# Kernel tuning notes

Hardware: AMD Instinct MI355X
Metric: run time of the kernel (lower is better)

Reference implementation:

```python
import jax, jax.numpy as jnp
import numpy as np

PATCH = 16  # conv kernel size == stride


def _patch_embed(im, W, b):
    # im: (B, C, H, W) NCHW; W: (hidden, C, s, s); returns (B, h, w, hidden)
    out = jax.lax.conv_general_dilated(
        im, W, window_strides=(PATCH, PATCH), padding='VALID',
        dimension_numbers=('NCHW', 'OIHW', 'NCHW'))
    out = out + b[None, :, None, None]
    return jnp.transpose(out, (0, 2, 3, 1))  # (B, h, w, hidden)


def setup_inputs() -> dict:
    key = jax.random.key(0)
    k1, k2, k3, k4 = jax.random.split(key, 4)
    B, C, H, Wd = 64, 3, 224, 224
    hidden = 384
    x = jax.random.normal(k1, (B, C, H, Wd), dtype=jnp.float32)
    y = jax.random.normal(k2, (B, C, H, Wd), dtype=jnp.float32)
    fan_in = C * PATCH * PATCH
    bound = 1.0 / np.sqrt(fan_in)
    W = jax.random.uniform(k3, (hidden, C, PATCH, PATCH), dtype=jnp.float32,
                           minval=-bound, maxval=bound)
    b = jax.random.uniform(k4, (hidden,), dtype=jnp.float32,
                           minval=-bound, maxval=bound)
    return {'x': x, 'y': y, 'W': W, 'b': b}


def reference(x, y, W, b):
    B = x.shape[0]
    xp = _patch_embed(x, W, b)  # (B, h, w, C)
    yp = _patch_embed(y, W, b)  # (B, h, w, C)
    h, w = xp.shape[1], xp.shape[2]
    logp = jax.nn.log_softmax(xp, axis=-1)          # (B, h, w, C)
    q = jax.lax.stop_gradient(jax.nn.softmax(yp, axis=-1))  # detached targets
    # CE[i, j] = mean over (h, w) of -(q_j * logp_i).sum(-1)
    # Faithful factorization of the (B, B, h, w, C) broadcast in the original.
    CE = -jnp.einsum('ihwc,jhwc->ij', logp, q) / (h * w)  # (B, B)
    close = jnp.trace(CE) / B
    far = (CE.sum() - jnp.trace(CE)) / (B * B - B)
    return close / far
```

## Files before the change

### kernel.cpp

```cpp
#include <hip/hip_runtime.h>

#define HID   384
#define K_PE  768
#define IMGST 150528

typedef unsigned short ushort_t;
using f32x4  = __attribute__((ext_vector_type(4))) float;
using short8 = __attribute__((ext_vector_type(8))) short;

__device__ __forceinline__ unsigned bfpack(float lo, float hi) {
    union { float f; unsigned u; } a, b; a.f = lo; b.f = hi;
    unsigned ra = (a.u + 0x7fffu + ((a.u >> 16) & 1u)) >> 16;
    unsigned rb = (b.u + 0x7fffu + ((b.u >> 16) & 1u)) & 0xffff0000u;
    return ra | rb;
}

__global__ __launch_bounds__(256) void prep(const float* __restrict__ W,
                                            ushort_t* __restrict__ Wfrag,
                                            float* __restrict__ scal) {
    const int t = blockIdx.x * 256 + threadIdx.x;
    if (t < 4) scal[t] = 0.f;
    const int n  = t / 96;
    const int ko = t % 96;
    const float4 a = *(const float4*)(W + (size_t)n * K_PE + ko * 8);
    const float4 b = *(const float4*)(W + (size_t)n * K_PE + ko * 8 + 4);
    uint4 p;
    p.x = bfpack(a.x, a.y); p.y = bfpack(a.z, a.w);
    p.z = bfpack(b.x, b.y); p.w = bfpack(b.z, b.w);
    const int nt   = n >> 4;
    const int kc   = ko >> 2;
    const int lane = (ko & 3) * 16 + (n & 15);
    ((uint4*)Wfrag)[(nt * 24 + kc) * 64 + lane] = p;
}

__global__ __launch_bounds__(512, 2) void pe_all(
    const float* __restrict__ xin, const float* __restrict__ yin,
    const ushort_t* __restrict__ Wfrag, const float* __restrict__ bias,
    float* __restrict__ scal, float* __restrict__ out) {
    const int p  = blockIdx.x;
    const int pi = p / 14;
    const int pj = p - pi * 14;

    __shared__ __align__(16) ushort_t Asx[2][64 * 64];
    __shared__ __align__(16) ushort_t Asy[2][64 * 64];
    __shared__ float Smx[8][32], Ssx[8][32], Smy[8][32], Ssy[8][32];
    __shared__ float LcL[2][HID], LcQ[2][HID];
    __shared__ float sT[8], sS[8];

    const int tid  = threadIdx.x;
    const int wave = tid >> 6;
    const int lane = tid & 63;
    const int lm   = lane & 15;
    const int lq   = lane >> 4;
    const int mg   = wave >> 2;
    const int nw   = wave & 3;
    const int wn   = nw * 96;

    const int sm = tid >> 3;
    const int qt = tid & 7;
    const float* abx = xin + (size_t)sm * IMGST + pi * 3584 + pj * 16;
    const float* aby = yin + (size_t)sm * IMGST + pi * 3584 + pj * 16;
    const int awoff = sm * 64 + ((qt ^ (sm & 7)) * 8);

    int ard[2][2];
#pragma unroll
    for (int ks = 0; ks < 2; ++ks)
#pragma unroll
        for (int mi = 0; mi < 2; ++mi)
            ard[ks][mi] = (mg * 32 + mi * 16 + lm) * 64 +
                          (((ks * 4 + lq) ^ (lm & 7)) * 8);

    const ushort_t* bbase = Wfrag + (size_t)lane * 8;

    f32x4 accx[2][6] = {};
    f32x4 accy[2][6] = {};

#define STAGE(KB, BUF)                                                       \
    {                                                                        \
        const int k0  = (KB) + qt * 8;                                       \
        const int off = (k0 >> 8) * 50176 + (((k0 >> 4) & 15) * 224) + (k0 & 15); \
        float4 f0 = *(const float4*)(abx + off);                             \
        float4 f1 = *(const float4*)(abx + off + 4);                         \
        float4 g0 = *(const float4*)(aby + off);                             \
        float4 g1 = *(const float4*)(aby + off + 4);                         \
        uint4 px, py;                                                        \
        px.x = bfpack(f0.x, f0.y); px.y = bfpack(f0.z, f0.w);                \
        px.z = bfpack(f1.x, f1.y); px.w = bfpack(f1.z, f1.w);                \
        py.x = bfpack(g0.x, g0.y); py.y = bfpack(g0.z, g0.w);                \
        py.z = bfpack(g1.x, g1.y); py.w = bfpack(g1.z, g1.w);                \
        *(uint4*)&Asx[BUF][awoff] = px;                                      \
        *(uint4*)&Asy[BUF][awoff] = py;                                      \
    }

    STAGE(0, 0)
    __syncthreads();

    for (int kbi = 0; kbi < 12; ++kbi) {
        const int cur = kbi & 1;
        if (kbi < 11) STAGE(kbi * 64 + 64, cur ^ 1)
#pragma unroll
        for (int ks = 0; ks < 2; ++ks) {
            short8 bfr[6], afx[2], afy[2];
#pragma unroll
            for (int ni = 0; ni < 6; ++ni)
                bfr[ni] = *(const short8*)(bbase +
                          (size_t)(((nw * 6 + ni) * 24 + kbi * 2 + ks) * 64) * 8);
#pragma unroll
            for (int mi = 0; mi < 2; ++mi) {
                afx[mi] = *(const short8*)&Asx[cur][ard[ks][mi]];
                afy[mi] = *(const short8*)&Asy[cur][ard[ks][mi]];
            }
#pragma unroll
            for (int mi = 0; mi < 2; ++mi)
#pragma unroll
                for (int ni = 0; ni < 6; ++ni) {
                    accx[mi][ni] = __builtin_amdgcn_mfma_f32_16x16x32_bf16(
                        afx[mi], bfr[ni], accx[mi][ni], 0, 0, 0);
                    accy[mi][ni] = __builtin_amdgcn_mfma_f32_16x16x32_bf16(
                        afy[mi], bfr[ni], accy[mi][ni], 0, 0, 0);
                }
        }
        __syncthreads();
    }
#undef STAGE

#pragma unroll
    for (int ni = 0; ni < 6; ++ni) {
        const float bv = bias[wn + ni * 16 + lm];
#pragma unroll
        for (int mi = 0; mi < 2; ++mi)
#pragma unroll
            for (int r = 0; r < 4; ++r) {
                accx[mi][ni][r] += bv;
                accy[mi][ni][r] += bv;
            }
    }

    float mx[2][4], my_[2][4];
#pragma unroll
    for (int mi = 0; mi < 2; ++mi)
#pragma unroll
        for (int r = 0; r < 4; ++r) {
            float a = accx[mi][0][r], b = accy[mi][0][r];
#pragma unroll
            for (int ni = 1; ni < 6; ++ni) {
                a = fmaxf(a, accx[mi][ni][r]);
                b = fmaxf(b, accy[mi][ni][r]);
            }
            mx[mi][r] = a; my_[mi][r] = b;
        }
#pragma unroll
    for (int off = 1; off < 16; off <<= 1)
#pragma unroll
        for (int mi = 0; mi < 2; ++mi)
#pragma unroll
            for (int r = 0; r < 4; ++r) {
                mx[mi][r]  = fmaxf(mx[mi][r],  __shfl_xor(mx[mi][r],  off));
                my_[mi][r] = fmaxf(my_[mi][r], __shfl_xor(my_[mi][r], off));
            }
    if (lm == 0)
#pragma unroll
        for (int mi = 0; mi < 2; ++mi)
#pragma unroll
            for (int r = 0; r < 4; ++r) {
                Smx[wave][mi * 16 + lq * 4 + r] = mx[mi][r];
                Smy[wave][mi * 16 + lq * 4 + r] = my_[mi][r];
            }
    __syncthreads();
#pragma unroll
    for (int mi = 0; mi < 2; ++mi)
#pragma unroll
        for (int r = 0; r < 4; ++r) {
            const int row = mi * 16 + lq * 4 + r;
            mx[mi][r]  = fmaxf(fmaxf(Smx[mg * 4 + 0][row], Smx[mg * 4 + 1][row]),
                               fmaxf(Smx[mg * 4 + 2][row], Smx[mg * 4 + 3][row]));
            my_[mi][r] = fmaxf(fmaxf(Smy[mg * 4 + 0][row], Smy[mg * 4 + 1][row]),
                               fmaxf(Smy[mg * 4 + 2][row], Smy[mg * 4 + 3][row]));
        }

    float sx[2][4], sy[2][4];
#pragma unroll
    for (int mi = 0; mi < 2; ++mi)
#pragma unroll
        for (int r = 0; r < 4; ++r) {
            float a = 0.f, b = 0.f;
#pragma unroll
            for (int ni = 0; ni < 6; ++ni) {
                a += __expf(accx[mi][ni][r] - mx[mi][r]);
                b += __expf(accy[mi][ni][r] - my_[mi][r]);
            }
            sx[mi][r] = a; sy[mi][r] = b;
        }
#pragma unroll
    for (int off = 1; off < 16; off <<= 1)
#pragma unroll
        for (int mi = 0; mi < 2; ++mi)
#pragma unroll
            for (int r = 0; r < 4; ++r) {
                sx[mi][r] += __shfl_xor(sx[mi][r], off);
                sy[mi][r] += __shfl_xor(sy[mi][r], off);
            }
    if (lm == 0)
#pragma unroll
        for (int mi = 0; mi < 2; ++mi)
#pragma unroll
            for (int r = 0; r < 4; ++r) {
                Ssx[wave][mi * 16 + lq * 4 + r] = sx[mi][r];
                Ssy[wave][mi * 16 + lq * 4 + r] = sy[mi][r];
            }
    __syncthreads();
#pragma unroll
    for (int mi = 0; mi < 2; ++mi)
#pragma unroll
        for (int r = 0; r < 4; ++r) {
            const int row = mi * 16 + lq * 4 + r;
            const float ssx = Ssx[mg * 4 + 0][row] + Ssx[mg * 4 + 1][row] +
                              Ssx[mg * 4 + 2][row] + Ssx[mg * 4 + 3][row];
            const float ssy = Ssy[mg * 4 + 0][row] + Ssy[mg * 4 + 1][row] +
                              Ssy[mg * 4 + 2][row] + Ssy[mg * 4 + 3][row];
            sx[mi][r] = mx[mi][r] + __logf(ssx);
            sy[mi][r] = 1.f / ssy;
        }

    float T = 0.f;
    float cL[6], cQ[6];
#pragma unroll
    for (int ni = 0; ni < 6; ++ni) { cL[ni] = 0.f; cQ[ni] = 0.f; }
#pragma unroll
    for (int mi = 0; mi < 2; ++mi)
#pragma unroll
        for (int r = 0; r < 4; ++r) {
            const float sh  = sx[mi][r];
            const float m   = my_[mi][r];
            const float inv = sy[mi][r];
#pragma unroll
            for (int ni = 0; ni < 6; ++ni) {
                const float lp = accx[mi][ni][r] - sh;
                const float qv = __expf(accy[mi][ni][r] - m) * inv;
                T += lp * qv;
                cL[ni] += lp;
                cQ[ni] += qv;
            }
        }
#pragma unroll
    for (int ni = 0; ni < 6; ++ni) {
        cL[ni] += __shfl_xor(cL[ni], 16); cL[ni] += __shfl_xor(cL[ni], 32);
        cQ[ni] += __shfl_xor(cQ[ni], 16); cQ[ni] += __shfl_xor(cQ[ni], 32);
    }
    if (lq == 0)
#pragma unroll
        for (int ni = 0; ni < 6; ++ni) {
            LcL[mg][wn + ni * 16 + lm] = cL[ni];
            LcQ[mg][wn + ni * 16 + lm] = cQ[ni];
        }
#pragma unroll
    for (int off = 32; off > 0; off >>= 1) T += __shfl_xor(T, off);
    if (lane == 0) sT[wave] = T;
    __syncthreads();

    float sp = 0.f;
    if (tid < HID) {
        const float L = LcL[0][tid] + LcL[1][tid];
        const float Q = LcQ[0][tid] + LcQ[1][tid];
        sp = L * Q;
    }
#pragma unroll
    for (int off = 32; off > 0; off >>= 1) sp += __shfl_xor(sp, off);
    if (lane == 0) sS[wave] = sp;
    __syncthreads();

    if (tid == 0) {
        float Tb = sT[0] + sT[1] + sT[2] + sT[3] + sT[4] + sT[5] + sT[6] + sT[7];
        float Sb = sS[0] + sS[1] + sS[2] + sS[3] + sS[4] + sS[5] + sS[6] + sS[7];
        atomicAdd(&scal[0], Tb);
        atomicAdd(&scal[1], Sb);
        __threadfence();
        int old = atomicAdd((int*)&scal[3], 1);
        if (old == (int)gridDim.x - 1) {
            float Tt = atomicAdd(&scal[0], 0.f);
            float St = atomicAdd(&scal[1], 0.f);
            out[0] = 63.f * Tt / (St - Tt);
        }
    }
}

extern "C" void kernel_launch(void* const* d_in, const int* in_sizes, int n_in,
                              void* d_out, int out_size, void* d_ws, size_t ws_size,
                              hipStream_t stream) {
    const float* x = (const float*)d_in[0];
    const float* y = (const float*)d_in[1];
    const float* W = (const float*)d_in[2];
    const float* b = (const float*)d_in[3];
    float* out = (float*)d_out;

    float*    scal  = (float*)d_ws;
    ushort_t* Wfrag = (ushort_t*)(scal + 16);

    prep<<<144, 256, 0, stream>>>(W, Wfrag, scal);
    pe_all<<<196, 512, 0, stream>>>(x, y, Wfrag, b, scal, out);
}
```

Before: 146.2 us.

## Split patch-embed blocks over batch sub-tiles and add a reduction kernel

The main kernel now launches four times as many smaller blocks: each block handles 16 batch rows of one patch position with 256 threads instead of all 64 rows with 512 threads. The goal is to fill more of the CUs than 196 large blocks can. Per-channel column sums of logp and q are written to global scratch, and a new finish kernel combines the four sub-blocks, forms the L·Q cross term and computes the final ratio. Staging is also changed so each thread loads one matrix (x or y) and the bf16 pack plus LDS store happen after the MFMAs, which hides global-load latency. In exchange there is an extra kernel launch and scratch traffic, and every weight fragment is reloaded by four times as many blocks.

```diff
diff --git a/kernel.cpp b/kernel.cpp
--- a/kernel.cpp
+++ b/kernel.cpp
@@ -3,6 +3,7 @@
 #define HID   384
 #define K_PE  768
 #define IMGST 150528
+#define MSUB  16
 
 typedef unsigned short ushort_t;
 using f32x4  = __attribute__((ext_vector_type(4))) float;
@@ -33,215 +34,187 @@
     ((uint4*)Wfrag)[(nt * 24 + kc) * 64 + lane] = p;
 }
 
-__global__ __launch_bounds__(512, 2) void pe_all(
+__global__ __launch_bounds__(256, 3) void pe_all(
     const float* __restrict__ xin, const float* __restrict__ yin,
     const ushort_t* __restrict__ Wfrag, const float* __restrict__ bias,
-    float* __restrict__ scal, float* __restrict__ out) {
-    const int p  = blockIdx.x;
-    const int pi = p / 14;
-    const int pj = p - pi * 14;
-
-    __shared__ __align__(16) ushort_t Asx[2][64 * 64];
-    __shared__ __align__(16) ushort_t Asy[2][64 * 64];
-    __shared__ float Smx[8][32], Ssx[8][32], Smy[8][32], Ssy[8][32];
-    __shared__ float LcL[2][HID], LcQ[2][HID];
-    __shared__ float sT[8], sS[8];
+    float* __restrict__ scal, float* __restrict__ Lg, float* __restrict__ Qg) {
+    const int blk = blockIdx.x;
+    const int p   = blk >> 2;
+    const int sub = blk & 3;
+    const int pi  = p / 14;
+    const int pj  = p - pi * 14;
+
+    __shared__ __align__(16) ushort_t Asx[2][MSUB * 64];
+    __shared__ __align__(16) ushort_t Asy[2][MSUB * 64];
+    __shared__ float Smx[4][16], Ssx[4][16], Smy[4][16], Ssy[4][16];
+    __shared__ float sT[4];
 
     const int tid  = threadIdx.x;
     const int wave = tid >> 6;
     const int lane = tid & 63;
     const int lm   = lane & 15;
     const int lq   = lane >> 4;
-    const int mg   = wave >> 2;
-    const int nw   = wave & 3;
-    const int wn   = nw * 96;
-
-    const int sm = tid >> 3;
-    const int qt = tid & 7;
-    const float* abx = xin + (size_t)sm * IMGST + pi * 3584 + pj * 16;
-    const float* aby = yin + (size_t)sm * IMGST + pi * 3584 + pj * 16;
-    const int awoff = sm * 64 + ((qt ^ (sm & 7)) * 8);
-
-    int ard[2][2];
+
+    const int mat  = tid >> 7;
+    const int sidx = tid & 127;
+    const int srow = sidx & 15;
+    const int soct = sidx >> 4;
+    const float* sbase = (mat ? yin : xin) +
+        (size_t)(sub * MSUB + srow) * IMGST + pi * 3584 + pj * 16;
+    ushort_t (* const Adst)[MSUB * 64] = mat ? Asy : Asx;
+    const int woff = srow * 64 + ((soct ^ (srow & 7)) * 8);
+
+    int ard[2];
 #pragma unroll
     for (int ks = 0; ks < 2; ++ks)
-#pragma unroll
-        for (int mi = 0; mi < 2; ++mi)
-            ard[ks][mi] = (mg * 32 + mi * 16 + lm) * 64 +
-                          (((ks * 4 + lq) ^ (lm & 7)) * 8);
+        ard[ks] = lm * 64 + (((ks * 4 + lq) ^ (lm & 7)) * 8);
 
     const ushort_t* bbase = Wfrag + (size_t)lane * 8;
 
-    f32x4 accx[2][6] = {};
-    f32x4 accy[2][6] = {};
-
-#define STAGE(KB, BUF)                                                       \
-    {                                                                        \
-        const int k0  = (KB) + qt * 8;                                       \
-        const int off = (k0 >> 8) * 50176 + (((k0 >> 4) & 15) * 224) + (k0 & 15); \
-        float4 f0 = *(const float4*)(abx + off);                             \
-        float4 f1 = *(const float4*)(abx + off + 4);                         \
-        float4 g0 = *(const float4*)(aby + off);                             \
-        float4 g1 = *(const float4*)(aby + off + 4);                         \
-        uint4 px, py;                                                        \
-        px.x = bfpack(f0.x, f0.y); px.y = bfpack(f0.z, f0.w);                \
-        px.z = bfpack(f1.x, f1.y); px.w = bfpack(f1.z, f1.w);                \
-        py.x = bfpack(g0.x, g0.y); py.y = bfpack(g0.z, g0.w);                \
-        py.z = bfpack(g1.x, g1.y); py.w = bfpack(g1.z, g1.w);                \
-        *(uint4*)&Asx[BUF][awoff] = px;                                      \
-        *(uint4*)&Asy[BUF][awoff] = py;                                      \
-    }
-
-    STAGE(0, 0)
+    f32x4 accx[6] = {};
+    f32x4 accy[6] = {};
+
+    {
+        const int k0  = soct * 8;
+        const int off = (k0 >> 8) * 50176 + (((k0 >> 4) & 15) * 224) + (k0 & 15);
+        const float4 f0 = *(const float4*)(sbase + off);
+        const float4 f1 = *(const float4*)(sbase + off + 4);
+        uint4 px;
+        px.x = bfpack(f0.x, f0.y); px.y = bfpack(f0.z, f0.w);
+        px.z = bfpack(f1.x, f1.y); px.w = bfpack(f1.z, f1.w);
+        *(uint4*)&Adst[0][woff] = px;
+    }
     __syncthreads();
 
     for (int kbi = 0; kbi < 12; ++kbi) {
         const int cur = kbi & 1;
-        if (kbi < 11) STAGE(kbi * 64 + 64, cur ^ 1)
+        const int kn  = (kbi < 11) ? (kbi + 1) * 64 + soct * 8 : soct * 8;
+        const int off = (kn >> 8) * 50176 + (((kn >> 4) & 15) * 224) + (kn & 15);
+        const float4 f0 = *(const float4*)(sbase + off);
+        const float4 f1 = *(const float4*)(sbase + off + 4);
+
 #pragma unroll
         for (int ks = 0; ks < 2; ++ks) {
-            short8 bfr[6], afx[2], afy[2];
+            short8 bfr[6];
 #pragma unroll
             for (int ni = 0; ni < 6; ++ni)
                 bfr[ni] = *(const short8*)(bbase +
-                          (size_t)(((nw * 6 + ni) * 24 + kbi * 2 + ks) * 64) * 8);
-#pragma unroll
-            for (int mi = 0; mi < 2; ++mi) {
-                afx[mi] = *(const short8*)&Asx[cur][ard[ks][mi]];
-                afy[mi] = *(const short8*)&Asy[cur][ard[ks][mi]];
+                          (size_t)(((wave * 6 + ni) * 24 + kbi * 2 + ks) * 64) * 8);
+            const short8 afx = *(const short8*)&Asx[cur][ard[ks]];
+            const short8 afy = *(const short8*)&Asy[cur][ard[ks]];
+#pragma unroll
+            for (int ni = 0; ni < 6; ++ni) {
+                accx[ni] = __builtin_amdgcn_mfma_f32_16x16x32_bf16(
+                    afx, bfr[ni], accx[ni], 0, 0, 0);
+                accy[ni] = __builtin_amdgcn_mfma_f32_16x16x32_bf16(
+                    afy, bfr[ni], accy[ni], 0, 0, 0);
             }
-#pragma unroll
-            for (int mi = 0; mi < 2; ++mi)
-#pragma unroll
-                for (int ni = 0; ni < 6; ++ni) {
-                    accx[mi][ni] = __builtin_amdgcn_mfma_f32_16x16x32_bf16(
-                        afx[mi], bfr[ni], accx[mi][ni], 0, 0, 0);
-                    accy[mi][ni] = __builtin_amdgcn_mfma_f32_16x16x32_bf16(
-                        afy[mi], bfr[ni], accy[mi][ni], 0, 0, 0);
-                }
-        }
+        }
+
+        uint4 px;
+        px.x = bfpack(f0.x, f0.y); px.y = bfpack(f0.z, f0.w);
+        px.z = bfpack(f1.x, f1.y); px.w = bfpack(f1.z, f1.w);
+        *(uint4*)&Adst[cur ^ 1][woff] = px;
         __syncthreads();
     }
-#undef STAGE
 
 #pragma unroll
     for (int ni = 0; ni < 6; ++ni) {
-        const float bv = bias[wn + ni * 16 + lm];
-#pragma unroll
-        for (int mi = 0; mi < 2; ++mi)
-#pragma unroll
-            for (int r = 0; r < 4; ++r) {
-                accx[mi][ni][r] += bv;
-                accy[mi][ni][r] += bv;
-            }
-    }
-
-    float mx[2][4], my_[2][4];
-#pragma unroll
-    for (int mi = 0; mi < 2; ++mi)
-#pragma unroll
-        for (int r = 0; r < 4; ++r) {
-            float a = accx[mi][0][r], b = accy[mi][0][r];
-#pragma unroll
-            for (int ni = 1; ni < 6; ++ni) {
-                a = fmaxf(a, accx[mi][ni][r]);
-                b = fmaxf(b, accy[mi][ni][r]);
-            }
-            mx[mi][r] = a; my_[mi][r] = b;
-        }
+        const float bv = bias[wave * 96 + ni * 16 + lm];
+#pragma unroll
+        for (int r = 0; r < 4; ++r) {
+            accx[ni][r] += bv;
+            accy[ni][r] += bv;
+        }
+    }
+
+    float mx[4], my_[4];
+#pragma unroll
+    for (int r = 0; r < 4; ++r) {
+        float a = accx[0][r], b = accy[0][r];
+#pragma unroll
+        for (int ni = 1; ni < 6; ++ni) {
+            a = fmaxf(a, accx[ni][r]);
+            b = fmaxf(b, accy[ni][r]);
+        }
+        mx[r] = a; my_[r] = b;
+    }
 #pragma unroll
     for (int off = 1; off < 16; off <<= 1)
 #pragma unroll
-        for (int mi = 0; mi < 2; ++mi)
-#pragma unroll
-            for (int r = 0; r < 4; ++r) {
-                mx[mi][r]  = fmaxf(mx[mi][r],  __shfl_xor(mx[mi][r],  off));
-                my_[mi][r] = fmaxf(my_[mi][r], __shfl_xor(my_[mi][r], off));
-            }
+        for (int r = 0; r < 4; ++r) {
+            mx[r]  = fmaxf(mx[r],  __shfl_xor(mx[r],  off));
+            my_[r] = fmaxf(my_[r], __shfl_xor(my_[r], off));
+        }
     if (lm == 0)
 #pragma unroll
-        for (int mi = 0; mi < 2; ++mi)
-#pragma unroll
-            for (int r = 0; r < 4; ++r) {
-                Smx[wave][mi * 16 + lq * 4 + r] = mx[mi][r];
-                Smy[wave][mi * 16 + lq * 4 + r] = my_[mi][r];
-            }
-    __syncthreads();
-#pragma unroll
-    for (int mi = 0; mi < 2; ++mi)
-#pragma unroll
-        for (int r = 0; r < 4; ++r) {
-            const int row = mi * 16 + lq * 4 + r;
-            mx[mi][r]  = fmaxf(fmaxf(Smx[mg * 4 + 0][row], Smx[mg * 4 + 1][row]),
-                               fmaxf(Smx[mg * 4 + 2][row], Smx[mg * 4 + 3][row]));
-            my_[mi][r] = fmaxf(fmaxf(Smy[mg * 4 + 0][row], Smy[mg * 4 + 1][row]),
-                               fmaxf(Smy[mg * 4 + 2][row], Smy[mg * 4 + 3][row]));
-        }
-
-    float sx[2][4], sy[2][4];
-#pragma unroll
-    for (int mi = 0; mi < 2; ++mi)
-#pragma unroll
-        for (int r = 0; r < 4; ++r) {
-            float a = 0.f, b = 0.f;
-#pragma unroll
-            for (int ni = 0; ni < 6; ++ni) {
-                a += __expf(accx[mi][ni][r] - mx[mi][r]);
-                b += __expf(accy[mi][ni][r] - my_[mi][r]);
-            }
-            sx[mi][r] = a; sy[mi][r] = b;
-        }
+        for (int r = 0; r < 4; ++r) {
+            Smx[wave][lq * 4 + r] = mx[r];
+            Smy[wave][lq * 4 + r] = my_[r];
+        }
+    __syncthreads();
+#pragma unroll
+    for (int r = 0; r < 4; ++r) {
+        const int row = lq * 4 + r;
+        mx[r]  = fmaxf(fmaxf(Smx[0][row], Smx[1][row]),
+                       fmaxf(Smx[2][row], Smx[3][row]));
+        my_[r] = fmaxf(fmaxf(Smy[0][row], Smy[1][row]),
+                       fmaxf(Smy[2][row], Smy[3][row]));
+    }
+
+    float sx[4], sy[4];
+#pragma unroll
+    for (int r = 0; r < 4; ++r) {
+        float a = 0.f, b = 0.f;
+#pragma unroll
+        for (int ni = 0; ni < 6; ++ni) {
+            a += __expf(accx[ni][r] - mx[r]);
+            b += __expf(accy[ni][r] - my_[r]);
+        }
+        sx[r] = a; sy[r] = b;
+    }
 #pragma unroll
     for (int off = 1; off < 16; off <<= 1)
 #pragma unroll
-        for (int mi = 0; mi < 2; ++mi)
-#pragma unroll
-            for (int r = 0; r < 4; ++r) {
-                sx[mi][r] += __shfl_xor(sx[mi][r], off);
-                sy[mi][r] += __shfl_xor(sy[mi][r], off);
-            }
+        for (int r = 0; r < 4; ++r) {
+            sx[r] += __shfl_xor(sx[r], off);
+            sy[r] += __shfl_xor(sy[r], off);
+        }
     if (lm == 0)
 #pragma unroll
-        for (int mi = 0; mi < 2; ++mi)
-#pragma unroll
-            for (int r = 0; r < 4; ++r) {
-                Ssx[wave][mi * 16 + lq * 4 + r] = sx[mi][r];
-                Ssy[wave][mi * 16 + lq * 4 + r] = sy[mi][r];
-            }
-    __syncthreads();
-#pragma unroll
-    for (int mi = 0; mi < 2; ++mi)
-#pragma unroll
-        for (int r = 0; r < 4; ++r) {
-            const int row = mi * 16 + lq * 4 + r;
-            const float ssx = Ssx[mg * 4 + 0][row] + Ssx[mg * 4 + 1][row] +
-                              Ssx[mg * 4 + 2][row] + Ssx[mg * 4 + 3][row];
-            const float ssy = Ssy[mg * 4 + 0][row] + Ssy[mg * 4 + 1][row] +
-                              Ssy[mg * 4 + 2][row] + Ssy[mg * 4 + 3][row];
-            sx[mi][r] = mx[mi][r] + __logf(ssx);
-            sy[mi][r] = 1.f / ssy;
-        }
+        for (int r = 0; r < 4; ++r) {
+            Ssx[wave][lq * 4 + r] = sx[r];
+            Ssy[wave][lq * 4 + r] = sy[r];
+        }
+    __syncthreads();
+    float shx[4], invy[4];
+#pragma unroll
+    for (int r = 0; r < 4; ++r) {
+        const int row = lq * 4 + r;
+        const float ssx = Ssx[0][row] + Ssx[1][row] + Ssx[2][row] + Ssx[3][row];
+        const float ssy = Ssy[0][row] + Ssy[1][row] + Ssy[2][row] + Ssy[3][row];
+        shx[r]  = mx[r] + __logf(ssx);
+        invy[r] = 1.f / ssy;
+    }
 
     float T = 0.f;
     float cL[6], cQ[6];
 #pragma unroll
     for (int ni = 0; ni < 6; ++ni) { cL[ni] = 0.f; cQ[ni] = 0.f; }
 #pragma unroll
-    for (int mi = 0; mi < 2; ++mi)
-#pragma unroll
-        for (int r = 0; r < 4; ++r) {
-            const float sh  = sx[mi][r];
-            const float m   = my_[mi][r];
-            const float inv = sy[mi][r];
-#pragma unroll
-            for (int ni = 0; ni < 6; ++ni) {
-                const float lp = accx[mi][ni][r] - sh;
-                const float qv = __expf(accy[mi][ni][r] - m) * inv;
-                T += lp * qv;
-                cL[ni] += lp;
-                cQ[ni] += qv;
-            }
-        }
+    for (int r = 0; r < 4; ++r) {
+        const float sh  = shx[r];
+        const float m   = my_[r];
+        const float inv = invy[r];
+#pragma unroll
+        for (int ni = 0; ni < 6; ++ni) {
+            const float lp = accx[ni][r] - sh;
+            const float qv = __expf(accy[ni][r] - m) * inv;
+            T += lp * qv;
+            cL[ni] += lp;
+            cQ[ni] += qv;
+        }
+    }
 #pragma unroll
     for (int ni = 0; ni < 6; ++ni) {
         cL[ni] += __shfl_xor(cL[ni], 16); cL[ni] += __shfl_xor(cL[ni], 32);
@@ -250,36 +223,40 @@
     if (lq == 0)
 #pragma unroll
         for (int ni = 0; ni < 6; ++ni) {
-            LcL[mg][wn + ni * 16 + lm] = cL[ni];
-            LcQ[mg][wn + ni * 16 + lm] = cQ[ni];
+            Lg[(size_t)blk * HID + wave * 96 + ni * 16 + lm] = cL[ni];
+            Qg[(size_t)blk * HID + wave * 96 + ni * 16 + lm] = cQ[ni];
         }
 #pragma unroll
     for (int off = 32; off > 0; off >>= 1) T += __shfl_xor(T, off);
     if (lane == 0) sT[wave] = T;
     __syncthreads();
-
-    float sp = 0.f;
-    if (tid < HID) {
-        const float L = LcL[0][tid] + LcL[1][tid];
-        const float Q = LcQ[0][tid] + LcQ[1][tid];
-        sp = L * Q;
-    }
-#pragma unroll
-    for (int off = 32; off > 0; off >>= 1) sp += __shfl_xor(sp, off);
-    if (lane == 0) sS[wave] = sp;
-    __syncthreads();
-
-    if (tid == 0) {
-        float Tb = sT[0] + sT[1] + sT[2] + sT[3] + sT[4] + sT[5] + sT[6] + sT[7];
-        float Sb = sS[0] + sS[1] + sS[2] + sS[3] + sS[4] + sS[5] + sS[6] + sS[7];
-        atomicAdd(&scal[0], Tb);
-        atomicAdd(&scal[1], Sb);
+    if (tid == 0) atomicAdd(&scal[0], sT[0] + sT[1] + sT[2] + sT[3]);
+}
+
+__global__ __launch_bounds__(384) void finish(const float* __restrict__ Lg,
+                                              const float* __restrict__ Qg,
+                                              float* __restrict__ scal,
+                                              float* __restrict__ out) {
+    const int p = blockIdx.x;
+    const int c = threadIdx.x;
+    const size_t b0 = (size_t)(p * 4) * HID + c;
+    const float L = Lg[b0] + Lg[b0 + HID] + Lg[b0 + 2 * HID] + Lg[b0 + 3 * HID];
+    const float Q = Qg[b0] + Qg[b0 + HID] + Qg[b0 + 2 * HID] + Qg[b0 + 3 * HID];
+    float s = L * Q;
+#pragma unroll
+    for (int off = 32; off > 0; off >>= 1) s += __shfl_xor(s, off);
+    __shared__ float sw[6];
+    if ((c & 63) == 0) sw[c >> 6] = s;
+    __syncthreads();
+    if (c == 0) {
+        const float Sp = sw[0] + sw[1] + sw[2] + sw[3] + sw[4] + sw[5];
+        atomicAdd(&scal[1], Sp);
         __threadfence();
-        int old = atomicAdd((int*)&scal[3], 1);
-        if (old == (int)gridDim.x - 1) {
-            float Tt = atomicAdd(&scal[0], 0.f);
-            float St = atomicAdd(&scal[1], 0.f);
-            out[0] = 63.f * Tt / (St - Tt);
+        const int old = atomicAdd((int*)&scal[3], 1);
+        if (old == 195) {
+            const float T = atomicAdd(&scal[0], 0.f);
+            const float S = atomicAdd(&scal[1], 0.f);
+            out[0] = 63.f * T / (S - T);
         }
     }
 }
@@ -295,7 +272,10 @@
 
     float*    scal  = (float*)d_ws;
     ushort_t* Wfrag = (ushort_t*)(scal + 16);
+    float*    Lg    = (float*)(Wfrag + 294912);
+    float*    Qg    = Lg + (size_t)784 * HID;
 
     prep<<<144, 256, 0, stream>>>(W, Wfrag, scal);
-    pe_all<<<196, 512, 0, stream>>>(x, y, Wfrag, b, scal, out);
-}
+    pe_all<<<784, 256, 0, stream>>>(x, y, Wfrag, b, scal, Lg, Qg);
+    finish<<<196, 384, 0, stream>>>(Lg, Qg, scal, out);
+}
```

New measurement: 154.8 us. 1.06x slower.

## Pre-pack images to bf16 patch tiles and stream them into LDS asynchronously

Applied to the files above, without the earlier changes.

A new pack kernel converts both images to bf16 once, reading rows coalesced through shared memory, and writes them in a per-position, per-k-block tile layout. The main GEMM kernel then uses global_load_lds to copy these tiles straight into LDS. It also splits each patch position across two 256-thread blocks (392 blocks in total). Column sums are combined across the two halves with global atomics and a per-position last-block reduction. This replaces the strided fp32 gathers and the in-loop conversion, and gives more blocks for occupancy, at the cost of an extra write and read of about 38MB of bf16 data and extra atomics.

```diff
diff --git a/kernel.cpp b/kernel.cpp
--- a/kernel.cpp
+++ b/kernel.cpp
@@ -3,10 +3,18 @@
 #define HID   384
 #define K_PE  768
 #define IMGST 150528
+#define POS   196
 
 typedef unsigned short ushort_t;
 using f32x4  = __attribute__((ext_vector_type(4))) float;
 using short8 = __attribute__((ext_vector_type(8))) short;
+
+typedef unsigned __attribute__((address_space(1))) u32_g;
+typedef unsigned __attribute__((address_space(3))) u32_s;
+
+__device__ __forceinline__ void glds16(const void* g, void* l) {
+    __builtin_amdgcn_global_load_lds((const u32_g*)g, (u32_s*)l, 16, 0, 0);
+}
 
 __device__ __forceinline__ unsigned bfpack(float lo, float hi) {
     union { float f; unsigned u; } a, b; a.f = lo; b.f = hi;
@@ -15,81 +23,114 @@
     return ra | rb;
 }
 
-__global__ __launch_bounds__(256) void prep(const float* __restrict__ W,
-                                            ushort_t* __restrict__ Wfrag,
-                                            float* __restrict__ scal) {
-    const int t = blockIdx.x * 256 + threadIdx.x;
-    if (t < 4) scal[t] = 0.f;
-    const int n  = t / 96;
-    const int ko = t % 96;
-    const float4 a = *(const float4*)(W + (size_t)n * K_PE + ko * 8);
-    const float4 b = *(const float4*)(W + (size_t)n * K_PE + ko * 8 + 4);
-    uint4 p;
-    p.x = bfpack(a.x, a.y); p.y = bfpack(a.z, a.w);
-    p.z = bfpack(b.x, b.y); p.w = bfpack(b.z, b.w);
-    const int nt   = n >> 4;
-    const int kc   = ko >> 2;
-    const int lane = (ko & 3) * 16 + (n & 15);
-    ((uint4*)Wfrag)[(nt * 24 + kc) * 64 + lane] = p;
-}
-
-__global__ __launch_bounds__(512, 2) void pe_all(
-    const float* __restrict__ xin, const float* __restrict__ yin,
+__global__ __launch_bounds__(256) void pack(
+    const float* __restrict__ x, const float* __restrict__ y,
+    const float* __restrict__ W, ushort_t* __restrict__ Wfrag,
+    ushort_t* __restrict__ imx, ushort_t* __restrict__ imy,
+    float* __restrict__ scal, int* __restrict__ pcnt,
+    float* __restrict__ Lp, float* __restrict__ Qp) {
+    const int b   = blockIdx.x;
+    const int tid = threadIdx.x;
+
+    if (b >= 896) {
+        const int t = (b - 896) * 256 + tid;
+        if (t < 16)  scal[t] = 0.f;
+        if (t < POS) pcnt[t] = 0;
+        for (int i = t; i < POS * HID; i += 36864) { Lp[i] = 0.f; Qp[i] = 0.f; }
+        const int n  = t / 96;
+        const int ko = t - n * 96;
+        const float4 a  = *(const float4*)(W + (size_t)n * K_PE + ko * 8);
+        const float4 bb = *(const float4*)(W + (size_t)n * K_PE + ko * 8 + 4);
+        uint4 pq;
+        pq.x = bfpack(a.x, a.y);  pq.y = bfpack(a.z, a.w);
+        pq.z = bfpack(bb.x, bb.y); pq.w = bfpack(bb.z, bb.w);
+        const int nt    = n >> 4;
+        const int kc    = ko >> 2;
+        const int lanew = (ko & 3) * 16 + (n & 15);
+        ((uint4*)Wfrag)[(nt * 24 + kc) * 64 + lanew] = pq;
+        return;
+    }
+
+    const int pi  = b >> 6;
+    const int img = b & 63;
+    __shared__ __align__(16) ushort_t L[2][48 * 232];
+
+    const float* bx = x + (size_t)img * IMGST + pi * 3584;
+    const float* by = y + (size_t)img * IMGST + pi * 3584;
+
+    for (int i = tid; i < 2688; i += 256) {
+        const int row = i / 56;
+        const int c4  = i - row * 56;
+        const int c   = row >> 4, r = row & 15;
+        const size_t so = (size_t)c * 50176 + r * 224 + c4 * 4;
+        const float4 fx = *(const float4*)(bx + so);
+        const float4 fy = *(const float4*)(by + so);
+        uint2 px, py;
+        px.x = bfpack(fx.x, fx.y); px.y = bfpack(fx.z, fx.w);
+        py.x = bfpack(fy.x, fy.y); py.y = bfpack(fy.z, fy.w);
+        *(uint2*)&L[0][row * 232 + c4 * 4] = px;
+        *(uint2*)&L[1][row * 232 + c4 * 4] = py;
+    }
+    __syncthreads();
+
+    for (int u = tid; u < 1344; u += 256) {
+        const int pj  = u / 96;
+        const int oc  = u - pj * 96;
+        const int kbi = oc >> 3, o = oc & 7;
+        const int k0  = oc * 8;
+        const int c   = k0 >> 8, kh = (k0 >> 4) & 15, kw0 = k0 & 15;
+        const int loff = (c * 16 + kh) * 232 + pj * 16 + kw0;
+        const uint4 vx = *(const uint4*)&L[0][loff];
+        const uint4 vy = *(const uint4*)&L[1][loff];
+        const size_t d = ((size_t)((pi * 14 + pj) * 12 + kbi) * 64 + img) * 64 + o * 8;
+        *(uint4*)&imx[d] = vx;
+        *(uint4*)&imy[d] = vy;
+    }
+}
+
+__global__ __launch_bounds__(256, 3) void pe2(
+    const ushort_t* __restrict__ imx, const ushort_t* __restrict__ imy,
     const ushort_t* __restrict__ Wfrag, const float* __restrict__ bias,
-    float* __restrict__ scal, float* __restrict__ out) {
-    const int p  = blockIdx.x;
-    const int pi = p / 14;
-    const int pj = p - pi * 14;
-
-    __shared__ __align__(16) ushort_t Asx[2][64 * 64];
-    __shared__ __align__(16) ushort_t Asy[2][64 * 64];
-    __shared__ float Smx[8][32], Ssx[8][32], Smy[8][32], Ssy[8][32];
-    __shared__ float LcL[2][HID], LcQ[2][HID];
-    __shared__ float sT[8], sS[8];
+    float* __restrict__ scal, int* __restrict__ pcnt,
+    float* __restrict__ Lp, float* __restrict__ Qp, float* __restrict__ out) {
+    const int blk  = blockIdx.x;
+    const int p    = blk >> 1;
+    const int half = blk & 1;
+
+    __shared__ __align__(16) ushort_t As[2][4096];
+    __shared__ float Smx[4][32], Ssx[4][32], Smy[4][32], Ssy[4][32];
+    __shared__ float sT[4];
+    __shared__ int lastp;
 
     const int tid  = threadIdx.x;
     const int wave = tid >> 6;
     const int lane = tid & 63;
     const int lm   = lane & 15;
     const int lq   = lane >> 4;
-    const int mg   = wave >> 2;
-    const int nw   = wave & 3;
-    const int wn   = nw * 96;
-
-    const int sm = tid >> 3;
-    const int qt = tid & 7;
-    const float* abx = xin + (size_t)sm * IMGST + pi * 3584 + pj * 16;
-    const float* aby = yin + (size_t)sm * IMGST + pi * 3584 + pj * 16;
-    const int awoff = sm * 64 + ((qt ^ (sm & 7)) * 8);
+
+    const int simg = wave * 8 + (lane >> 3);
+    const int so   = (lane & 7) ^ ((lane >> 3) & 7);
+    const size_t sbyte = (size_t)p * 98304 +
+                         ((size_t)(half * 32 + simg)) * 128 + so * 16;
+    const char* gx = (const char*)imx + sbyte;
+    const char* gy = (const char*)imy + sbyte;
 
     int ard[2][2];
 #pragma unroll
     for (int ks = 0; ks < 2; ++ks)
 #pragma unroll
         for (int mi = 0; mi < 2; ++mi)
-            ard[ks][mi] = (mg * 32 + mi * 16 + lm) * 64 +
-                          (((ks * 4 + lq) ^ (lm & 7)) * 8);
+            ard[ks][mi] = (mi * 16 + lm) * 64 + (((ks * 4 + lq) ^ (lm & 7)) * 8);
 
     const ushort_t* bbase = Wfrag + (size_t)lane * 8;
 
     f32x4 accx[2][6] = {};
     f32x4 accy[2][6] = {};
 
-#define STAGE(KB, BUF)                                                       \
-    {                                                                        \
-        const int k0  = (KB) + qt * 8;                                       \
-        const int off = (k0 >> 8) * 50176 + (((k0 >> 4) & 15) * 224) + (k0 & 15); \
-        float4 f0 = *(const float4*)(abx + off);                             \
-        float4 f1 = *(const float4*)(abx + off + 4);                         \
-        float4 g0 = *(const float4*)(aby + off);                             \
-        float4 g1 = *(const float4*)(aby + off + 4);                         \
-        uint4 px, py;                                                        \
-        px.x = bfpack(f0.x, f0.y); px.y = bfpack(f0.z, f0.w);                \
-        px.z = bfpack(f1.x, f1.y); px.w = bfpack(f1.z, f1.w);                \
-        py.x = bfpack(g0.x, g0.y); py.y = bfpack(g0.z, g0.w);                \
-        py.z = bfpack(g1.x, g1.y); py.w = bfpack(g1.z, g1.w);                \
-        *(uint4*)&Asx[BUF][awoff] = px;                                      \
-        *(uint4*)&Asy[BUF][awoff] = py;                                      \
+#define STAGE(KB, BUF)                                       \
+    {                                                        \
+        glds16(gx + (size_t)(KB) * 8192, &As[BUF][wave * 512]);        \
+        glds16(gy + (size_t)(KB) * 8192, &As[BUF][2048 + wave * 512]); \
     }
 
     STAGE(0, 0)
@@ -97,18 +138,19 @@
 
     for (int kbi = 0; kbi < 12; ++kbi) {
         const int cur = kbi & 1;
-        if (kbi < 11) STAGE(kbi * 64 + 64, cur ^ 1)
 #pragma unroll
         for (int ks = 0; ks < 2; ++ks) {
-            short8 bfr[6], afx[2], afy[2];
+            short8 bfr[6];
 #pragma unroll
             for (int ni = 0; ni < 6; ++ni)
                 bfr[ni] = *(const short8*)(bbase +
-                          (size_t)(((nw * 6 + ni) * 24 + kbi * 2 + ks) * 64) * 8);
+                          (size_t)(((wave * 6 + ni) * 24 + kbi * 2 + ks) * 64) * 8);
+            if (ks == 0 && kbi < 11) STAGE(kbi + 1, cur ^ 1)
+            short8 afx[2], afy[2];
 #pragma unroll
             for (int mi = 0; mi < 2; ++mi) {
-                afx[mi] = *(const short8*)&Asx[cur][ard[ks][mi]];
-                afy[mi] = *(const short8*)&Asy[cur][ard[ks][mi]];
+                afx[mi] = *(const short8*)&As[cur][ard[ks][mi]];
+                afy[mi] = *(const short8*)&As[cur][2048 + ard[ks][mi]];
             }
 #pragma unroll
             for (int mi = 0; mi < 2; ++mi)
@@ -126,7 +168,7 @@
 
 #pragma unroll
     for (int ni = 0; ni < 6; ++ni) {
-        const float bv = bias[wn + ni * 16 + lm];
+        const float bv = bias[wave * 96 + ni * 16 + lm];
 #pragma unroll
         for (int mi = 0; mi < 2; ++mi)
 #pragma unroll
@@ -141,13 +183,13 @@
     for (int mi = 0; mi < 2; ++mi)
 #pragma unroll
         for (int r = 0; r < 4; ++r) {
-            float a = accx[mi][0][r], b = accy[mi][0][r];
+            float a = accx[mi][0][r], bb = accy[mi][0][r];
 #pragma unroll
             for (int ni = 1; ni < 6; ++ni) {
-                a = fmaxf(a, accx[mi][ni][r]);
-                b = fmaxf(b, accy[mi][ni][r]);
-            }
-            mx[mi][r] = a; my_[mi][r] = b;
+                a  = fmaxf(a,  accx[mi][ni][r]);
+                bb = fmaxf(bb, accy[mi][ni][r]);
+            }
+            mx[mi][r] = a; my_[mi][r] = bb;
         }
 #pragma unroll
     for (int off = 1; off < 16; off <<= 1)
@@ -172,10 +214,10 @@
 #pragma unroll
         for (int r = 0; r < 4; ++r) {
             const int row = mi * 16 + lq * 4 + r;
-            mx[mi][r]  = fmaxf(fmaxf(Smx[mg * 4 + 0][row], Smx[mg * 4 + 1][row]),
-                               fmaxf(Smx[mg * 4 + 2][row], Smx[mg * 4 + 3][row]));
-            my_[mi][r] = fmaxf(fmaxf(Smy[mg * 4 + 0][row], Smy[mg * 4 + 1][row]),
-                               fmaxf(Smy[mg * 4 + 2][row], Smy[mg * 4 + 3][row]));
+            mx[mi][r]  = fmaxf(fmaxf(Smx[0][row], Smx[1][row]),
+                               fmaxf(Smx[2][row], Smx[3][row]));
+            my_[mi][r] = fmaxf(fmaxf(Smy[0][row], Smy[1][row]),
+                               fmaxf(Smy[2][row], Smy[3][row]));
         }
 
     float sx[2][4], sy[2][4];
@@ -183,13 +225,13 @@
     for (int mi = 0; mi < 2; ++mi)
 #pragma unroll
         for (int r = 0; r < 4; ++r) {
-            float a = 0.f, b = 0.f;
+            float a = 0.f, bb = 0.f;
 #pragma unroll
             for (int ni = 0; ni < 6; ++ni) {
-                a += __expf(accx[mi][ni][r] - mx[mi][r]);
-                b += __expf(accy[mi][ni][r] - my_[mi][r]);
-            }
-            sx[mi][r] = a; sy[mi][r] = b;
+                a  += __expf(accx[mi][ni][r] - mx[mi][r]);
+                bb += __expf(accy[mi][ni][r] - my_[mi][r]);
+            }
+            sx[mi][r] = a; sy[mi][r] = bb;
         }
 #pragma unroll
     for (int off = 1; off < 16; off <<= 1)
@@ -209,17 +251,16 @@
                 Ssy[wave][mi * 16 + lq * 4 + r] = sy[mi][r];
             }
     __syncthreads();
+    float shx[2][4], invy[2][4];
 #pragma unroll
     for (int mi = 0; mi < 2; ++mi)
 #pragma unroll
         for (int r = 0; r < 4; ++r) {
             const int row = mi * 16 + lq * 4 + r;
-            const float ssx = Ssx[mg * 4 + 0][row] + Ssx[mg * 4 + 1][row] +
-                              Ssx[mg * 4 + 2][row] + Ssx[mg * 4 + 3][row];
-            const float ssy = Ssy[mg * 4 + 0][row] + Ssy[mg * 4 + 1][row] +
-                              Ssy[mg * 4 + 2][row] + Ssy[mg * 4 + 3][row];
-            sx[mi][r] = mx[mi][r] + __logf(ssx);
-            sy[mi][r] = 1.f / ssy;
+            const float ssx = Ssx[0][row] + Ssx[1][row] + Ssx[2][row] + Ssx[3][row];
+            const float ssy = Ssy[0][row] + Ssy[1][row] + Ssy[2][row] + Ssy[3][row];
+            shx[mi][r]  = mx[mi][r] + __logf(ssx);
+            invy[mi][r] = 1.f / ssy;
         }
 
     float T = 0.f;
@@ -230,9 +271,9 @@
     for (int mi = 0; mi < 2; ++mi)
 #pragma unroll
         for (int r = 0; r < 4; ++r) {
-            const float sh  = sx[mi][r];
+            const float sh  = shx[mi][r];
             const float m   = my_[mi][r];
-            const float inv = sy[mi][r];
+            const float inv = invy[mi][r];
 #pragma unroll
             for (int ni = 0; ni < 6; ++ni) {
                 const float lp = accx[mi][ni][r] - sh;
@@ -250,35 +291,41 @@
     if (lq == 0)
 #pragma unroll
         for (int ni = 0; ni < 6; ++ni) {
-            LcL[mg][wn + ni * 16 + lm] = cL[ni];
-            LcQ[mg][wn + ni * 16 + lm] = cQ[ni];
+            atomicAdd(&Lp[p * HID + wave * 96 + ni * 16 + lm], cL[ni]);
+            atomicAdd(&Qp[p * HID + wave * 96 + ni * 16 + lm], cQ[ni]);
         }
 #pragma unroll
     for (int off = 32; off > 0; off >>= 1) T += __shfl_xor(T, off);
     if (lane == 0) sT[wave] = T;
     __syncthreads();
-
-    float sp = 0.f;
-    if (tid < HID) {
-        const float L = LcL[0][tid] + LcL[1][tid];
-        const float Q = LcQ[0][tid] + LcQ[1][tid];
-        sp = L * Q;
-    }
-#pragma unroll
-    for (int off = 32; off > 0; off >>= 1) sp += __shfl_xor(sp, off);
-    if (lane == 0) sS[wave] = sp;
-    __syncthreads();
-
     if (tid == 0) {
-        float Tb = sT[0] + sT[1] + sT[2] + sT[3] + sT[4] + sT[5] + sT[6] + sT[7];
-        float Sb = sS[0] + sS[1] + sS[2] + sS[3] + sS[4] + sS[5] + sS[6] + sS[7];
-        atomicAdd(&scal[0], Tb);
-        atomicAdd(&scal[1], Sb);
+        atomicAdd(&scal[0], sT[0] + sT[1] + sT[2] + sT[3]);
         __threadfence();
-        int old = atomicAdd((int*)&scal[3], 1);
-        if (old == (int)gridDim.x - 1) {
-            float Tt = atomicAdd(&scal[0], 0.f);
-            float St = atomicAdd(&scal[1], 0.f);
+        const int old = atomicAdd(&pcnt[p], 1);
+        lastp = (old == 1);
+    }
+    __syncthreads();
+
+    if (lastp) {
+        float s = 0.f;
+        for (int c = tid; c < HID; c += 256) {
+            const float Lv = atomicAdd(&Lp[p * HID + c], 0.f);
+            const float Qv = atomicAdd(&Qp[p * HID + c], 0.f);
+            s += Lv * Qv;
+        }
+#pragma unroll
+        for (int off = 32; off > 0; off >>= 1) s += __shfl_xor(s, off);
+        if (lane == 0) sT[wave] = s;
+        __syncthreads();
+        if (tid == 0) atomicAdd(&scal[1], sT[0] + sT[1] + sT[2] + sT[3]);
+    }
+
+    if (tid == 0) {
+        __threadfence();
+        const int g = atomicAdd((int*)&scal[3], 1);
+        if (g == (int)gridDim.x - 1) {
+            const float Tt = atomicAdd(&scal[0], 0.f);
+            const float St = atomicAdd(&scal[1], 0.f);
             out[0] = 63.f * Tt / (St - Tt);
         }
     }
@@ -293,9 +340,15 @@
     const float* b = (const float*)d_in[3];
     float* out = (float*)d_out;
 
-    float*    scal  = (float*)d_ws;
-    ushort_t* Wfrag = (ushort_t*)(scal + 16);
-
-    prep<<<144, 256, 0, stream>>>(W, Wfrag, scal);
-    pe_all<<<196, 512, 0, stream>>>(x, y, Wfrag, b, scal, out);
-}
+    char* ws = (char*)d_ws;
+    float*    scal  = (float*)ws;
+    int*      pcnt  = (int*)(ws + 1024);
+    ushort_t* Wfrag = (ushort_t*)(ws + 2048);
+    float*    Lp    = (float*)(ws + 591872);
+    float*    Qp    = (float*)(ws + 892928);
+    ushort_t* imx   = (ushort_t*)(ws + 1196032);
+    ushort_t* imy   = (ushort_t*)(ws + 20463616);
+
+    pack<<<1040, 256, 0, stream>>>(x, y, W, Wfrag, imx, imy, scal, pcnt, Lp, Qp);
+    pe2<<<392, 256, 0, stream>>>(imx, imy, Wfrag, b, scal, pcnt, Lp, Qp, out);
+}
```

New measurement: 155.2 us. 1.06x slower.
